# Optimization experiments

Hardware: AMD Instinct MI355X
Metric: run time of the kernel (lower is better)

Reference implementation:

```python
import jax, jax.numpy as jnp
import numpy as np
import math

B, S, H, M, NH = 4, 1024, 1024, 32768, 1  # batch, seq, hidden, memory_size, num_heads


def setup_inputs() -> dict:
    key = jax.random.key(0)
    ks = jax.random.split(key, 12)
    init = lambda k, shape: (jax.random.normal(k, shape, dtype=jnp.float32) * 0.02)
    return {
        "hidden_states": jax.random.normal(ks[0], (B, S, H), dtype=jnp.float32),
        "Wq": init(ks[1], (H, H)), "bq": jnp.zeros((H,), jnp.float32),
        "Wk": init(ks[2], (H, H)), "bk": jnp.zeros((H,), jnp.float32),
        "Wv": init(ks[3], (H, H)), "bv": jnp.zeros((H,), jnp.float32),
        "Wo": init(ks[4], (H, H)), "bo": jnp.zeros((H,), jnp.float32),
        "memory_keys": init(ks[5], (NH, M, H)),
        "memory_values": init(ks[6], (NH, M, H)),
        "memory_age": jnp.zeros((NH, M), jnp.float32),
    }


def reference(hidden_states, Wq, bq, Wk, bk, Wv, bv, Wo, bo,
              memory_keys, memory_values, memory_age):
    b, s, _ = hidden_states.shape
    # projections (torch Linear: x @ W.T + b), split into heads
    q = (hidden_states @ Wq.T + bq).reshape(b, s, NH, -1)
    k = (hidden_states @ Wk.T + bk).reshape(b, s, NH, -1)
    v = (hidden_states @ Wv.T + bv).reshape(b, s, NH, -1)

    # cross-attention to external memory: [b,s,h,m]
    scores = jnp.einsum('bshd,hmd->bshm', q, memory_keys) / math.sqrt(H)
    probs = jax.nn.softmax(scores, axis=-1)  # dropout is identity (eval / p used deterministically)
    mem_out = jnp.einsum('bshm,hmd->bshd', probs, memory_values)

    # --- memory update (LRU-style topk scatter) ---
    age = memory_age + 1.0                       # [h,m]
    importance = probs.sum(axis=(0, 1))          # [h,m]
    _, upd_idx = jax.lax.top_k(age + (1.0 - importance), s)  # [h, s]
    h_idx = jnp.arange(NH)[:, None]              # [h,1]
    src_k = k[0, -1][:, None, :]                 # [h,1,d] -> broadcast over s slots
    src_v = v[0, -1][:, None, :]
    new_keys = memory_keys.at[h_idx, upd_idx].set(src_k)
    new_values = memory_values.at[h_idx, upd_idx].set(src_v)
    new_age = age.at[h_idx, upd_idx].set(0.0)

    output = mem_out.reshape(b, s, -1) @ Wo.T + bo

    access_counts = jnp.sum(probs > 0.01, axis=(0, 1))          # [h,m]
    max_scores = jnp.max(scores, axis=-1).mean()
    memory_usage = jnp.mean((new_age > 0).astype(jnp.float32))
    return (output, access_counts, max_scores, memory_usage,
            new_keys, new_values, new_age)
```

## Files before the change

### kernel.cpp

```cpp
#include <hip/hip_runtime.h>

#define SCALE 0.03125f
#define BAND_EPS 1e-6
#define BAND_CAP 8192
#define RB 4
#define NCHUNK 8

typedef unsigned int u32;
typedef unsigned short u16;
typedef unsigned long long u64;
typedef __attribute__((ext_vector_type(8))) short bf16x8;
typedef __attribute__((ext_vector_type(4))) float f32x4;

#define MFMA16(A,B,C) __builtin_amdgcn_mfma_f32_16x16x32_bf16(A,B,C,0,0,0)

__device__ __forceinline__ u32 fenc(float x){ u32 u=__float_as_uint(x); return (u&0x80000000u)? ~u : (u|0x80000000u); }
__device__ __forceinline__ float fdec(u32 e){ return (e&0x80000000u)? __uint_as_float(e&0x7FFFFFFFu) : __uint_as_float(~e); }
__device__ __forceinline__ u16 f2bf(float f){ u32 u=__float_as_uint(f); u32 r=(u + 0x7FFFu + ((u>>16)&1u))>>16; return (u16)r; }
__device__ __forceinline__ float bf2f(u16 h){ return __uint_as_float(((u32)h)<<16); }

__device__ __forceinline__ uint4 nt_load16(const void* p){
  const u64* q = (const u64*)p;
  u64 lo = __builtin_nontemporal_load(q);
  u64 hi = __builtin_nontemporal_load(q+1);
  uint4 r;
  r.x = (u32)lo; r.y = (u32)(lo>>32);
  r.z = (u32)hi; r.w = (u32)(hi>>32);
  return r;
}

__global__ __launch_bounds__(256) void k_projq64(const float* __restrict__ X, const float* __restrict__ W,
    const float* __restrict__ bias, float* __restrict__ Qhi, u16* __restrict__ Qh, u16* __restrict__ Ql)
{
  __shared__ float Xs[16][68], Ws[16][68];
  int t=threadIdx.x, ty=t>>4, tx=t&15;
  int row0=blockIdx.y*64, col0=blockIdx.x*64;
  int lr=t>>2, lk=(t&3)*4;
  double acc[4][4]={};
  for (int k0=0;k0<1024;k0+=16){
    __syncthreads();
    {
      float4 x = *(const float4*)(X + (size_t)(row0+lr)*1024 + k0 + lk);
      float4 w = *(const float4*)(W + (size_t)(col0+lr)*1024 + k0 + lk);
      Xs[lk+0][lr]=x.x; Xs[lk+1][lr]=x.y; Xs[lk+2][lr]=x.z; Xs[lk+3][lr]=x.w;
      Ws[lk+0][lr]=w.x; Ws[lk+1][lr]=w.y; Ws[lk+2][lr]=w.z; Ws[lk+3][lr]=w.w;
    }
    __syncthreads();
    #pragma unroll
    for (int kk=0;kk<16;kk++){
      double a[4], b[4];
      #pragma unroll
      for (int i=0;i<4;i++) a[i] = (double)Xs[kk][ty*4+i];
      #pragma unroll
      for (int j=0;j<4;j++) b[j] = (double)Ws[kk][tx*4+j];
      #pragma unroll
      for (int i=0;i<4;i++)
        #pragma unroll
        for (int j=0;j<4;j++)
          acc[i][j] = fma(a[i], b[j], acc[i][j]);
    }
  }
  #pragma unroll
  for (int i=0;i<4;i++)
    #pragma unroll
    for (int j=0;j<4;j++){
      double q = acc[i][j] + (double)bias[col0+tx*4+j];
      float hi = (float)q;
      size_t off = (size_t)(row0+ty*4+i)*1024 + col0 + tx*4 + j;
      Qhi[off] = hi;
      if (Qh){
        u16 h = f2bf(hi);
        Qh[off] = h;
        Ql[off] = f2bf(hi - bf2f(h));
      }
    }
}

__global__ __launch_bounds__(256) void k_rowproj(const float* __restrict__ hs,
    const float* __restrict__ Wk, const float* __restrict__ bk,
    const float* __restrict__ Wv, const float* __restrict__ bv,
    float* __restrict__ krow, float* __restrict__ vrow)
{
  int b = blockIdx.x; int which = b >> 10; int o = b & 1023; int t = threadIdx.x;
  const float* W = which ? Wv : Wk;
  const float* bias = which ? bv : bk;
  const float* x = hs + (size_t)1023*1024;
  double s = 0;
  for (int k=t;k<1024;k+=256) s += (double)x[k] * (double)W[(size_t)o*1024+k];
  __shared__ double sd[256];
  sd[t]=s; __syncthreads();
  for (int off=128;off>0;off>>=1){ if(t<off) sd[t]+=sd[t+off]; __syncthreads(); }
  if (t==0){ float* dst = which? vrow : krow; dst[o] = (float)(sd[0] + (double)bias[o]); }
}

__global__ __launch_bounds__(256) void k_cvt_mk(const float* __restrict__ src, u16* __restrict__ dst)
{
  size_t base = ((size_t)blockIdx.x*256 + threadIdx.x) * 16;
  float v[16];
  #pragma unroll
  for (int q=0;q<4;q++) *(float4*)&v[q*4] = *(const float4*)(src + base + q*4);
  u16 h[16];
  #pragma unroll
  for (int q=0;q<16;q++) h[q] = f2bf(v[q]);
  *(uint4*)(dst+base)   = *(uint4*)&h[0];
  *(uint4*)(dst+base+8) = *(uint4*)&h[8];
}

__global__ __launch_bounds__(256) void k_cvt_mvt(const float* __restrict__ MV, u32* __restrict__ MVT)
{
  size_t mp = blockIdx.x; int d = threadIdx.x*4;
  float4 r0 = *(const float4*)(MV + (2*mp  )*1024 + d);
  float4 r1 = *(const float4*)(MV + (2*mp+1)*1024 + d);
  u32 o[4];
  o[0] = (u32)f2bf(r0.x) | ((u32)f2bf(r1.x)<<16);
  o[1] = (u32)f2bf(r0.y) | ((u32)f2bf(r1.y)<<16);
  o[2] = (u32)f2bf(r0.z) | ((u32)f2bf(r1.z)<<16);
  o[3] = (u32)f2bf(r0.w) | ((u32)f2bf(r1.w)<<16);
  *(uint4*)(MVT + mp*1024 + d) = *(uint4*)o;
}

template<bool SPLIT>
__device__ __forceinline__ void sweep_core(
    const float* __restrict__ Qg, const float* __restrict__ MKg,
    int row0, int col0,
    u16 (*Ah)[40], u16 (*Al)[40], u16 (*Bh)[40],
    f32x4 acc[2][8])
{
  int t = threadIdx.x;
  int w = t >> 6, g = (t >> 4) & 3, c = t & 15;
  int srow = t >> 1, sq = (t & 1) * 16;
  const float* xg = Qg  + (size_t)(row0 + srow)*1024 + sq;
  const float* wg = MKg + (size_t)(col0 + srow)*1024 + sq;
  float xr[16], wr[16];
  #pragma unroll
  for (int q=0;q<4;q++){
    *(float4*)&xr[q*4] = *(const float4*)(xg + q*4);
    *(float4*)&wr[q*4] = *(const float4*)(wg + q*4);
  }
  for (int k0 = 0; k0 < 1024; k0 += 32){
    u16 ah[16], al[16], bh[16];
    #pragma unroll
    for (int q=0;q<16;q++){
      u16 h = f2bf(xr[q]); ah[q]=h;
      bh[q] = f2bf(wr[q]);
      if constexpr (SPLIT) al[q]=f2bf(xr[q]-bf2f(h));
    }
    __syncthreads();
    *(uint4*)&Ah[srow][sq]   = *(uint4*)&ah[0];
    *(uint4*)&Ah[srow][sq+8] = *(uint4*)&ah[8];
    *(uint4*)&Bh[srow][sq]   = *(uint4*)&bh[0];
    *(uint4*)&Bh[srow][sq+8] = *(uint4*)&bh[8];
    if constexpr (SPLIT){
      *(uint4*)&Al[srow][sq]   = *(uint4*)&al[0];
      *(uint4*)&Al[srow][sq+8] = *(uint4*)&al[8];
    }
    __syncthreads();
    if (k0 + 32 < 1024){
      #pragma unroll
      for (int q=0;q<4;q++){
        *(float4*)&xr[q*4] = *(const float4*)(xg + k0+32 + q*4);
        *(float4*)&wr[q*4] = *(const float4*)(wg + k0+32 + q*4);
      }
    }
    bf16x8 afh[2], afl[2];
    #pragma unroll
    for (int fi=0; fi<2; fi++){
      afh[fi] = *(const bf16x8*)&Ah[w*32 + fi*16 + c][g*8];
      if constexpr (SPLIT) afl[fi] = *(const bf16x8*)&Al[w*32 + fi*16 + c][g*8];
    }
    #pragma unroll
    for (int fj=0; fj<8; fj++){
      bf16x8 bfh = *(const bf16x8*)&Bh[fj*16 + c][g*8];
      #pragma unroll
      for (int fi=0; fi<2; fi++){
        acc[fi][fj] = MFMA16(afh[fi], bfh, acc[fi][fj]);
        if constexpr (SPLIT)
          acc[fi][fj] = MFMA16(afl[fi], bfh, acc[fi][fj]);
      }
    }
  }
}

template<bool SPLIT>
__device__ __forceinline__ void sweep_core_pre(
    const u16* __restrict__ Ag, const u16* __restrict__ Alg, const u16* __restrict__ Bg,
    int row0, int col0,
    u16 (*Ah)[40], u16 (*Al)[40], u16 (*Bh)[40],
    f32x4 acc[2][8])
{
  int t = threadIdx.x;
  int w = t >> 6, g = (t >> 4) & 3, c = t & 15;
  int srow = t >> 1, sq = (t & 1) * 16;
  const u16* xa = Ag + (size_t)(row0+srow)*1024 + sq;
  const u16* wb = Bg + (size_t)(col0+srow)*1024 + sq;
  const u16* xl = Alg + (size_t)(row0+srow)*1024 + sq;
  uint4 a0 = *(const uint4*)xa, a1 = *(const uint4*)(xa+8);
  uint4 b0 = *(const uint4*)wb, b1 = *(const uint4*)(wb+8);
  uint4 l0, l1;
  if constexpr (SPLIT){ l0 = *(const uint4*)xl; l1 = *(const uint4*)(xl+8); }
  for (int k0 = 0; k0 < 1024; k0 += 32){
    __syncthreads();
    *(uint4*)&Ah[srow][sq]   = a0;
    *(uint4*)&Ah[srow][sq+8] = a1;
    *(uint4*)&Bh[srow][sq]   = b0;
    *(uint4*)&Bh[srow][sq+8] = b1;
    if constexpr (SPLIT){
      *(uint4*)&Al[srow][sq]   = l0;
      *(uint4*)&Al[srow][sq+8] = l1;
    }
    __syncthreads();
    if (k0 + 32 < 1024){
      a0=*(const uint4*)(xa+k0+32); a1=*(const uint4*)(xa+k0+40);
      b0=*(const uint4*)(wb+k0+32); b1=*(const uint4*)(wb+k0+40);
      if constexpr (SPLIT){ l0=*(const uint4*)(xl+k0+32); l1=*(const uint4*)(xl+k0+40); }
    }
    bf16x8 afh[2], afl[2];
    #pragma unroll
    for (int fi=0; fi<2; fi++){
      afh[fi] = *(const bf16x8*)&Ah[w*32 + fi*16 + c][g*8];
      if constexpr (SPLIT) afl[fi] = *(const bf16x8*)&Al[w*32 + fi*16 + c][g*8];
    }
    #pragma unroll
    for (int fj=0; fj<8; fj++){
      bf16x8 bfh = *(const bf16x8*)&Bh[fj*16 + c][g*8];
      #pragma unroll
      for (int fi=0; fi<2; fi++){
        acc[fi][fj] = MFMA16(afh[fi], bfh, acc[fi][fj]);
        if constexpr (SPLIT)
          acc[fi][fj] = MFMA16(afl[fi], bfh, acc[fi][fj]);
      }
    }
  }
}

__device__ __forceinline__ void sweep1_epi(f32x4 acc[2][8], int row0,
    double* Zrow, u32* rmk)
{
  int t=threadIdx.x, w=t>>6, g=(t>>4)&3, c=t&15;
  #pragma unroll
  for (int fi=0;fi<2;fi++){
    #pragma unroll
    for (int r=0;r<4;r++){
      float mx=-1e30f, sm=0.f;
      #pragma unroll
      for (int fj=0;fj<8;fj++){
        float sc = acc[fi][fj][r]*SCALE;
        mx = fmaxf(mx, sc);
        sm += expf(sc);
      }
      #pragma unroll
      for (int o=1;o<16;o<<=1){
        mx = fmaxf(mx, __shfl_xor(mx,o,64));
        sm += __shfl_xor(sm,o,64);
      }
      if (c==0){
        int row = row0 + w*32 + fi*16 + g*4 + r;
        atomicMax(&rmk[row], fenc(mx));
        atomicAdd(&Zrow[row], (double)sm);
      }
    }
  }
}

__global__ __launch_bounds__(256) void k_sweep1m(const float* __restrict__ Q,
    const float* __restrict__ MK, double* __restrict__ Zrow, u32* __restrict__ rmk)
{
  __shared__ __align__(16) u16 ldsbuf[2*128*40];
  u16 (*Ah)[40]=(u16(*)[40])(ldsbuf);
  u16 (*Bh)[40]=(u16(*)[40])(ldsbuf+128*40);
  int row0=blockIdx.y*128, col0=blockIdx.x*128;
  f32x4 acc[2][8];
  #pragma unroll
  for (int fi=0;fi<2;fi++)
    #pragma unroll
    for (int fj=0;fj<8;fj++) acc[fi][fj] = (f32x4){0.f,0.f,0.f,0.f};
  sweep_core<false>(Q, MK, row0, col0, Ah, Ah, Bh, acc);
  sweep1_epi(acc, row0, Zrow, rmk);
}

__global__ __launch_bounds__(256) void k_sweep1p(const u16* __restrict__ Qh,
    const u16* __restrict__ MKh, double* __restrict__ Zrow, u32* __restrict__ rmk)
{
  __shared__ __align__(16) u16 ldsbuf[2*128*40];
  u16 (*Ah)[40]=(u16(*)[40])(ldsbuf);
  u16 (*Bh)[40]=(u16(*)[40])(ldsbuf+128*40);
  int row0=blockIdx.y*128, col0=blockIdx.x*128;
  f32x4 acc[2][8];
  #pragma unroll
  for (int fi=0;fi<2;fi++)
    #pragma unroll
    for (int fj=0;fj<8;fj++) acc[fi][fj] = (f32x4){0.f,0.f,0.f,0.f};
  sweep_core_pre<false>(Qh, Qh, MKh, row0, col0, Ah, Ah, Bh, acc);
  sweep1_epi(acc, row0, Zrow, rmk);
}

__global__ __launch_bounds__(256) void k_invz(const double* __restrict__ Z, const u32* __restrict__ rmk,
    float* __restrict__ invZ, double* __restrict__ invZd, float* __restrict__ rowmax)
{
  int r = blockIdx.x*256 + threadIdx.x;
  double iz = 1.0 / Z[r];
  invZ[r] = (float)iz;
  invZd[r] = iz;
  rowmax[r] = fdec(rmk[r]);
}

__device__ __forceinline__ void sweep2_epi(f32x4 acc[2][8], int row0, int col0,
    const float* invZ, double* imp, int* cnt, u16* P, u16* ldsbuf)
{
  int t=threadIdx.x, w=t>>6, g=(t>>4)&3, c=t&15;
  double colp[8]={0,0,0,0,0,0,0,0};
  int    colc[8]={0,0,0,0,0,0,0,0};
  #pragma unroll
  for (int fi=0;fi<2;fi++){
    float iz[4];
    #pragma unroll
    for (int r=0;r<4;r++) iz[r] = invZ[row0 + w*32 + fi*16 + g*4 + r];
    #pragma unroll
    for (int fj=0;fj<8;fj++){
      #pragma unroll
      for (int r=0;r<4;r++){
        float p = expf(acc[fi][fj][r]*SCALE)*iz[r];
        int row = row0 + w*32 + fi*16 + g*4 + r;
        __builtin_nontemporal_store(f2bf(p), &P[(size_t)row*32768 + col0 + fj*16 + c]);
        colp[fj] += (double)p;
        colc[fj] += (p > 0.01f) ? 1 : 0;
      }
    }
  }
  __syncthreads();
  double (*red)[128] = (double(*)[128])ldsbuf;
  #pragma unroll
  for (int fj=0;fj<8;fj++) red[w*4+g][fj*16+c] = colp[fj];
  __syncthreads();
  if (t < 128){
    double s=0;
    #pragma unroll
    for (int q=0;q<16;q++) s += red[q][t];
    atomicAdd(&imp[col0+t], s);
  }
  __syncthreads();
  #pragma unroll
  for (int fj=0;fj<8;fj++) red[w*4+g][fj*16+c] = (double)colc[fj];
  __syncthreads();
  if (t < 128){
    double s=0;
    #pragma unroll
    for (int q=0;q<16;q++) s += red[q][t];
    int ci = (int)(s+0.5);
    if (ci) atomicAdd(&cnt[col0+t], ci);
  }
}

__global__ __launch_bounds__(256) void k_sweep2m(const float* __restrict__ Q,
    const float* __restrict__ MK, const float* __restrict__ invZ,
    double* __restrict__ imp, int* __restrict__ cnt, u16* __restrict__ P)
{
  __shared__ __align__(16) u16 ldsbuf[3*128*40];
  u16 (*Ah)[40]=(u16(*)[40])(ldsbuf);
  u16 (*Al)[40]=(u16(*)[40])(ldsbuf+128*40);
  u16 (*Bh)[40]=(u16(*)[40])(ldsbuf+2*128*40);
  int row0=blockIdx.y*128, col0=blockIdx.x*128;
  f32x4 acc[2][8];
  #pragma unroll
  for (int fi=0;fi<2;fi++)
    #pragma unroll
    for (int fj=0;fj<8;fj++) acc[fi][fj] = (f32x4){0.f,0.f,0.f,0.f};
  sweep_core<true>(Q, MK, row0, col0, Ah, Al, Bh, acc);
  sweep2_epi(acc, row0, col0, invZ, imp, cnt, P, ldsbuf);
}

__global__ __launch_bounds__(256) void k_sweep2p(const u16* __restrict__ Qh,
    const u16* __restrict__ Ql, const u16* __restrict__ MKh, const float* __restrict__ invZ,
    double* __restrict__ imp, int* __restrict__ cnt, u16* __restrict__ P)
{
  __shared__ __align__(16) u16 ldsbuf[3*128*40];
  u16 (*Ah)[40]=(u16(*)[40])(ldsbuf);
  u16 (*Al)[40]=(u16(*)[40])(ldsbuf+128*40);
  u16 (*Bh)[40]=(u16(*)[40])(ldsbuf+2*128*40);
  int row0=blockIdx.y*128, col0=blockIdx.x*128;
  f32x4 acc[2][8];
  #pragma unroll
  for (int fi=0;fi<2;fi++)
    #pragma unroll
    for (int fj=0;fj<8;fj++) acc[fi][fj] = (f32x4){0.f,0.f,0.f,0.f};
  sweep_core_pre<true>(Qh, Ql, MKh, row0, col0, Ah, Al, Bh, acc);
  sweep2_epi(acc, row0, col0, invZ, imp, cnt, P, ldsbuf);
}

template<int MODE>
__global__ __launch_bounds__(1024) void k_select(const double* __restrict__ imp,
    const float* __restrict__ mage, double* __restrict__ vsout, int* __restrict__ sel)
{
  __shared__ int hist[256];
  __shared__ int scanbuf[1024];
  __shared__ u32 s_digit; __shared__ int s_rr;
  int t = threadIdx.x;
  int m0 = t*32;
  u32 key[32];
  #pragma unroll
  for (int i=0;i<32;i++){
    int m = m0+i;
    float v = (mage[m] + 1.0f) + (1.0f - (float)imp[m]);
    key[i] = fenc(v);
  }
  u32 prefix = 0, pmask = 0;
  int rr = 1024;
  for (int pass=0; pass<4; pass++){
    int shift = 24 - pass*8;
    if (t<256) hist[t]=0;
    __syncthreads();
    #pragma unroll
    for (int i=0;i<32;i++){
      if ((key[i] & pmask) == prefix)
        atomicAdd(&hist[(key[i]>>shift)&255u], 1);
    }
    __syncthreads();
    if (t==0){
      int cum=0; int d=255;
      for (; d>0; d--){
        if (cum + hist[d] >= rr) break;
        cum += hist[d];
      }
      s_rr = rr - cum;
      s_digit = (u32)d;
    }
    __syncthreads();
    rr = s_rr;
    prefix |= (s_digit << shift);
    pmask  |= (255u << shift);
    __syncthreads();
  }
  u32 keystar = prefix;
  int krem = rr;
  if (MODE==0){
    if (t==0) *vsout = (double)fdec(keystar);
    return;
  }
  int lc = 0;
  #pragma unroll
  for (int i=0;i<32;i++) lc += (key[i]==keystar) ? 1 : 0;
  scanbuf[t] = lc;
  __syncthreads();
  for (int off=1; off<1024; off<<=1){
    int v_ = scanbuf[t];
    int add = (t>=off)? scanbuf[t-off] : 0;
    __syncthreads();
    scanbuf[t] = v_ + add;
    __syncthreads();
  }
  int run = scanbuf[t] - lc;
  #pragma unroll
  for (int i=0;i<32;i++){
    int s_;
    if (key[i] > keystar) s_ = 1;
    else if (key[i] == keystar){ s_ = (run < krem) ? 1 : 0; run++; }
    else s_ = 0;
    sel[m0+i] = s_;
  }
}

__global__ __launch_bounds__(256) void k_band(const double* __restrict__ imp,
    const float* __restrict__ mage, const double* __restrict__ vsp,
    int* __restrict__ bandcnt, int* __restrict__ bandidx)
{
  int m = blockIdx.x*256 + threadIdx.x;
  double v = ((double)mage[m] + 1.0) + (1.0 - imp[m]);
  double vs = *vsp;
  if (fabs(v - vs) <= BAND_EPS){
    int idx = atomicAdd(bandcnt, 1);
    if (idx < BAND_CAP) bandidx[idx] = m;
  }
}

__global__ __launch_bounds__(256) void k_repair2(const int* __restrict__ bandcnt, const int* __restrict__ bandidx,
    const float* __restrict__ Qhi, const float* __restrict__ MK,
    const double* __restrict__ invZd, double* __restrict__ partial)
{
  int bc = *bandcnt; if (bc > BAND_CAP) bc = BAND_CAP;
  int s0 = blockIdx.x * RB;
  if (s0 >= bc) return;
  int ns = bc - s0; if (ns > RB) ns = RB;
  int r0 = blockIdx.y * 512;
  __shared__ float mks[RB][1024];
  __shared__ double izl[512];
  __shared__ double red[256];
  int t = threadIdx.x;
  for (int idx = t; idx < RB*1024; idx += 256){
    int j = idx >> 10, d = idx & 1023;
    mks[j][d] = (j < ns) ? MK[(size_t)bandidx[s0+j]*1024 + d] : 0.f;
  }
  for (int r = t; r < 512; r += 256) izl[r] = invZd[r0 + r];
  __syncthreads();
  int wave = t>>6, lane = t&63, d0 = lane*16, sl = lane&3;
  double mkr[RB][16];
  #pragma unroll
  for (int j=0;j<RB;j++)
    #pragma unroll
    for (int q=0;q<16;q++) mkr[j][q] = (double)mks[j][d0+q];
  double acc = 0;
  for (int rr = wave; rr < 512; rr += 4){
    const float4* hp = (const float4*)(Qhi + (size_t)(r0+rr)*1024 + d0);
    float4 h0=hp[0], h1=hp[1], h2=hp[2], h3=hp[3];
    double hh[16]={h0.x,h0.y,h0.z,h0.w,h1.x,h1.y,h1.z,h1.w,
                   h2.x,h2.y,h2.z,h2.w,h3.x,h3.y,h3.z,h3.w};
    double p[RB];
    #pragma unroll
    for (int j=0;j<RB;j++){
      double a0=0, a1=0;
      #pragma unroll
      for (int q=0;q<8;q++){
        a0 = fma(hh[2*q],   mkr[j][2*q],   a0);
        a1 = fma(hh[2*q+1], mkr[j][2*q+1], a1);
      }
      p[j] = a0 + a1;
    }
    #pragma unroll
    for (int o=1;o<16;o<<=1)
      #pragma unroll
      for (int j=0;j<RB;j++) p[j] += __shfl_xor(p[j], o, 64);
    double v = (sl==0)? p[0] : (sl==1)? p[1] : (sl==2)? p[2] : p[3];
    v += __shfl_xor(v, 16, 64);
    v += __shfl_xor(v, 32, 64);
    acc += exp(v * (1.0/32.0)) * izl[rr];
  }
  red[t] = acc;
  __syncthreads();
  for (int o=128; o>=RB; o>>=1){
    if (t < o) red[t] += red[t+o];
    __syncthreads();
  }
  if (t < ns) partial[(size_t)(s0+t)*NCHUNK + blockIdx.y] = red[t];
}

__global__ __launch_bounds__(256) void k_repair_fin(const int* __restrict__ bandcnt,
    const int* __restrict__ bandidx, const double* __restrict__ partial, double* __restrict__ imp)
{
  int bc = *bandcnt; if (bc > BAND_CAP) bc = BAND_CAP;
  int slot = blockIdx.x*256 + threadIdx.x;
  if (slot >= bc) return;
  double s = 0;
  #pragma unroll
  for (int ch=0; ch<NCHUNK; ch++) s += partial[(size_t)slot*NCHUNK + ch];
  imp[bandidx[slot]] = s * 0.0625;
}

__global__ __launch_bounds__(256) void k_pvm(const u16* __restrict__ P,
    const float* __restrict__ MV, float* __restrict__ O)
{
  __shared__ __align__(16) u16 Ap[128][40];
  __shared__ u32 Bv[16][132];
  int t=threadIdx.x, w=t>>6, g=(t>>4)&3, c=t&15;
  int row0=blockIdx.x*128, d0=blockIdx.y*128;
  size_t kb0 = (size_t)blockIdx.z*8192;
  int srow=t>>1, sq=(t&1)*16;
  int mp=t>>5, dc=t&31;
  f32x4 acc[2][8];
  #pragma unroll
  for (int fi=0;fi<2;fi++)
    #pragma unroll
    for (int fj=0;fj<8;fj++) acc[fi][fj] = (f32x4){0.f,0.f,0.f,0.f};
  const u16*  pg  = P  + (size_t)(row0+srow)*32768 + kb0 + sq;
  const float* mva = MV + (kb0 + 2*mp  )*1024 + d0 + dc;
  const float* mvb = mva + 1024;
  const float* mvc = mva + 16*1024;
  const float* mvd = mvc + 1024;
  uint4 pa0 = *(const uint4*)pg;
  uint4 pa1 = *(const uint4*)(pg + 8);
  float a0[4], b0[4], a1[4], b1[4];
  #pragma unroll
  for (int j=0;j<4;j++){ a0[j]=mva[32*j]; b0[j]=mvb[32*j]; a1[j]=mvc[32*j]; b1[j]=mvd[32*j]; }
  for (int kt=0; kt<256; kt++){
    __syncthreads();
    *(uint4*)&Ap[srow][sq]   = pa0;
    *(uint4*)&Ap[srow][sq+8] = pa1;
    #pragma unroll
    for (int j=0;j<4;j++){
      Bv[mp  ][dc+32*j] = (u32)f2bf(a0[j]) | ((u32)f2bf(b0[j])<<16);
      Bv[mp+8][dc+32*j] = (u32)f2bf(a1[j]) | ((u32)f2bf(b1[j])<<16);
    }
    __syncthreads();
    if (kt+1 < 256){
      size_t ko = (size_t)(kt+1)*32;
      pa0 = *(const uint4*)(pg + ko);
      pa1 = *(const uint4*)(pg + ko + 8);
      size_t fo = ko*1024;
      #pragma unroll
      for (int j=0;j<4;j++){
        a0[j]=mva[fo+32*j]; b0[j]=mvb[fo+32*j];
        a1[j]=mvc[fo+32*j]; b1[j]=mvd[fo+32*j];
      }
    }
    bf16x8 af[2];
    af[0] = *(const bf16x8*)&Ap[w*32 + c][g*8];
    af[1] = *(const bf16x8*)&Ap[w*32 + 16 + c][g*8];
    #pragma unroll
    for (int fj=0; fj<8; fj++){
      union { u32 u[4]; bf16x8 v; } bb;
      #pragma unroll
      for (int qq=0; qq<4; qq++) bb.u[qq] = Bv[4*g+qq][fj*16 + c];
      acc[0][fj] = MFMA16(af[0], bb.v, acc[0][fj]);
      acc[1][fj] = MFMA16(af[1], bb.v, acc[1][fj]);
    }
  }
  #pragma unroll
  for (int fi=0;fi<2;fi++)
    #pragma unroll
    for (int fj=0;fj<8;fj++)
      #pragma unroll
      for (int r=0;r<4;r++)
        atomicAdd(&O[(size_t)(row0 + w*32 + fi*16 + g*4 + r)*1024 + d0 + fj*16 + c],
                  acc[fi][fj][r]);
}

__global__ __launch_bounds__(256) void k_pvmp(const u16* __restrict__ P,
    const u32* __restrict__ MVT, float* __restrict__ O)
{
  __shared__ __align__(16) u16 Ap[128][40];
  __shared__ u32 Bv[16][132];
  int t=threadIdx.x, w=t>>6, g=(t>>4)&3, c=t&15;
  int row0=blockIdx.x*128, d0=blockIdx.y*128;
  size_t kb0 = (size_t)blockIdx.z*8192;
  size_t pb0 = kb0 >> 1;
  int srow=t>>1, sq=(t&1)*16;
  int mp=t>>5, dc=t&31;
  f32x4 acc[2][8];
  #pragma unroll
  for (int fi=0;fi<2;fi++)
    #pragma unroll
    for (int fj=0;fj<8;fj++) acc[fi][fj] = (f32x4){0.f,0.f,0.f,0.f};
  const u16* pg   = P   + (size_t)(row0+srow)*32768 + kb0 + sq;
  const u32* mvt0 = MVT + (pb0 + mp    )*1024 + d0 + dc;
  const u32* mvt1 = MVT + (pb0 + 8 + mp)*1024 + d0 + dc;
  uint4 pa0 = nt_load16(pg);
  uint4 pa1 = nt_load16(pg + 8);
  u32 b0[4], b1[4];
  #pragma unroll
  for (int j=0;j<4;j++){ b0[j]=mvt0[32*j]; b1[j]=mvt1[32*j]; }
  for (int kt=0; kt<256; kt++){
    __syncthreads();
    *(uint4*)&Ap[srow][sq]   = pa0;
    *(uint4*)&Ap[srow][sq+8] = pa1;
    #pragma unroll
    for (int j=0;j<4;j++){
      Bv[mp  ][dc+32*j] = b0[j];
      Bv[mp+8][dc+32*j] = b1[j];
    }
    __syncthreads();
    if (kt+1 < 256){
      size_t ko = (size_t)(kt+1)*32;
      pa0 = nt_load16(pg + ko);
      pa1 = nt_load16(pg + ko + 8);
      size_t fo = (size_t)(kt+1)*16*1024;
      #pragma unroll
      for (int j=0;j<4;j++){ b0[j]=mvt0[fo+32*j]; b1[j]=mvt1[fo+32*j]; }
    }
    bf16x8 af[2];
    af[0] = *(const bf16x8*)&Ap[w*32 + c][g*8];
    af[1] = *(const bf16x8*)&Ap[w*32 + 16 + c][g*8];
    #pragma unroll
    for (int fj=0; fj<8; fj++){
      union { u32 u[4]; bf16x8 v; } bb;
      #pragma unroll
      for (int qq=0; qq<4; qq++) bb.u[qq] = Bv[4*g+qq][fj*16 + c];
      acc[0][fj] = MFMA16(af[0], bb.v, acc[0][fj]);
      acc[1][fj] = MFMA16(af[1], bb.v, acc[1][fj]);
    }
  }
  #pragma unroll
  for (int fi=0;fi<2;fi++)
    #pragma unroll
    for (int fj=0;fj<8;fj++)
      #pragma unroll
      for (int r=0;r<4;r++)
        atomicAdd(&O[(size_t)(row0 + w*32 + fi*16 + g*4 + r)*1024 + d0 + fj*16 + c],
                  acc[fi][fj][r]);
}

__global__ __launch_bounds__(256) void k_projm(const float* __restrict__ X,
    const float* __restrict__ W, const float* __restrict__ bias, float* __restrict__ Y)
{
  __shared__ __align__(16) u16 ldsbuf[2*128*40];
  u16 (*Ah)[40]=(u16(*)[40])(ldsbuf);
  u16 (*Bh)[40]=(u16(*)[40])(ldsbuf+128*40);
  int t=threadIdx.x, w=t>>6, g=(t>>4)&3, c=t&15;
  int row0=blockIdx.y*128, col0=blockIdx.x*128;
  f32x4 acc[2][8];
  #pragma unroll
  for (int fi=0;fi<2;fi++)
    #pragma unroll
    for (int fj=0;fj<8;fj++) acc[fi][fj] = (f32x4){0.f,0.f,0.f,0.f};
  sweep_core<false>(X, W, row0, col0, Ah, Ah, Bh, acc);
  #pragma unroll
  for (int fi=0;fi<2;fi++)
    #pragma unroll
    for (int fj=0;fj<8;fj++){
      float bb = bias[col0 + fj*16 + c];
      #pragma unroll
      for (int r=0;r<4;r++)
        Y[(size_t)(row0 + w*32 + fi*16 + g*4 + r)*1024 + col0 + fj*16 + c]
          = acc[fi][fj][r] + bb;
    }
}

__global__ __launch_bounds__(256) void k_scatter(const float* __restrict__ mk, const float* __restrict__ mv,
    const float* __restrict__ mage, const float* __restrict__ krow, const float* __restrict__ vrow,
    const int* __restrict__ sel, float* __restrict__ nk, float* __restrict__ nv,
    float* __restrict__ na, int* __restrict__ usage)
{
  int s = blockIdx.x, t = threadIdx.x;
  bool is = sel[s] != 0;
  const float2* sk = (const float2*)krow;
  const float2* sv = (const float2*)vrow;
  const float2* ok = (const float2*)(mk + (size_t)s*1024);
  const float2* ov = (const float2*)(mv + (size_t)s*1024);
  float2* dk = (float2*)(nk + (size_t)s*1024);
  float2* dv = (float2*)(nv + (size_t)s*1024);
  #pragma unroll
  for (int q=t;q<512;q+=256){
    dk[q] = is ? sk[q] : ok[q];
    dv[q] = is ? sv[q] : ov[q];
  }
  if (t==0){
    float a = mage[s] + 1.0f;
    float nav = is ? 0.0f : a;
    na[s] = nav;
    if (nav > 0.0f) atomicAdd(usage, 1);
  }
}

__global__ __launch_bounds__(256) void k_fin(const float* __restrict__ rowmax, const int* __restrict__ cnt,
    const int* __restrict__ usage, float* __restrict__ acc_out, float* __restrict__ scal)
{
  int t = threadIdx.x;
  __shared__ double sd[256];
  double s = 0;
  for (int r=t;r<4096;r+=256) s += (double)rowmax[r];
  sd[t]=s; __syncthreads();
  for (int o=128;o>0;o>>=1){ if (t<o) sd[t]+=sd[t+o]; __syncthreads(); }
  if (t==0){
    scal[0] = (float)(sd[0] / 4096.0);
    scal[1] = (float)((double)(*usage) / 32768.0);
  }
  for (int m=t;m<32768;m+=256) acc_out[m] = (float)cnt[m];
}

extern "C" void kernel_launch(void* const* d_in, const int* in_sizes, int n_in,
                              void* d_out, int out_size, void* d_ws, size_t ws_size,
                              hipStream_t stream) {
  const float* hs  = (const float*)d_in[0];
  const float* Wq  = (const float*)d_in[1];
  const float* bq  = (const float*)d_in[2];
  const float* Wk  = (const float*)d_in[3];
  const float* bk  = (const float*)d_in[4];
  const float* Wv  = (const float*)d_in[5];
  const float* bv  = (const float*)d_in[6];
  const float* Wo  = (const float*)d_in[7];
  const float* bo  = (const float*)d_in[8];
  const float* mk  = (const float*)d_in[9];
  const float* mv  = (const float*)d_in[10];
  const float* mage= (const float*)d_in[11];
  float* out = (float*)d_out;

  char* ws = (char*)d_ws;
  const size_t MB = 1024*1024;
  bool fast = ws_size >= 82*MB;
  size_t stats_off = fast ? 80*MB : 16*MB;
  char* st = ws + stats_off;

  double* Zrow   = (double*)(st);
  u32*    rmk    = (u32*)  (st + 32768);
  float*  invZ   = (float*)(st + 49152);
  double* invZd  = (double*)(st + 65536);
  float*  rowmax = (float*)(st + 98304);
  double* imp    = (double*)(st + 114688);
  int*    cnt    = (int*)  (st + 376832);
  int*    sel    = (int*)  (st + 507904);
  float*  krow   = (float*)(st + 638976);
  float*  vrow   = (float*)(st + 643072);
  int*    usage  = (int*)  (st + 647168);
  double* vstar  = (double*)(st + 647176);
  int*    bandcnt= (int*)  (st + 647184);
  int*    bandidx= (int*)  (st + 647188);
  double* partial= (double*)(st + 680960);

  float* O   = (float*)ws;
  u16*   Qh  = (u16*)ws;
  u16*   Ql  = (u16*)(ws + 8*MB);
  u16*   MKh = (u16*)(ws + 16*MB);
  u32*   MVT = (u32*)(ws + 16*MB);

  float* Qhi = (float*)d_out;
  u16*   P   = (u16*)((char*)d_out + 16908544);

  dim3 blk(256);
  if (fast){
    hipMemsetAsync(st, 0, 647188 + BAND_CAP*4, stream);
    k_projq64<<<dim3(16,64),blk,0,stream>>>(hs, Wq, bq, Qhi, Qh, Ql);
    k_cvt_mk<<<8192,blk,0,stream>>>(mk, MKh);
    k_rowproj<<<2048,blk,0,stream>>>(hs, Wk, bk, Wv, bv, krow, vrow);
    k_sweep1p<<<dim3(256,32),blk,0,stream>>>(Qh, MKh, Zrow, rmk);
    k_invz<<<16,blk,0,stream>>>(Zrow, rmk, invZ, invZd, rowmax);
    k_sweep2p<<<dim3(256,32),blk,0,stream>>>(Qh, Ql, MKh, invZ, imp, cnt, P);
    hipMemsetAsync(ws, 0, 16*MB, stream);
    k_cvt_mvt<<<16384,blk,0,stream>>>(mv, MVT);
    k_select<0><<<1,1024,0,stream>>>(imp, mage, vstar, nullptr);
    k_band<<<128,blk,0,stream>>>(imp, mage, vstar, bandcnt, bandidx);
    k_repair2<<<dim3(BAND_CAP/RB, NCHUNK),blk,0,stream>>>(bandcnt, bandidx, Qhi, mk, invZd, partial);
    k_repair_fin<<<BAND_CAP/256,blk,0,stream>>>(bandcnt, bandidx, partial, imp);
    k_pvmp<<<dim3(32,8,4),blk,0,stream>>>(P, MVT, O);
    k_projm<<<dim3(8,32),blk,0,stream>>>(O, Wo, bo, out);
    k_select<1><<<1,1024,0,stream>>>(imp, mage, nullptr, sel);
    k_scatter<<<32768,blk,0,stream>>>(mk, mv, mage, krow, vrow, sel,
        out + 4227074, out + 37781506, out + 71335938, usage);
    k_fin<<<1,blk,0,stream>>>(rowmax, cnt, usage, out + 4194304, out + 4227072);
  } else {
    hipMemsetAsync(ws, 0, 16*MB + 647188 + BAND_CAP*4, stream);
    k_projq64<<<dim3(16,64),blk,0,stream>>>(hs, Wq, bq, Qhi, nullptr, nullptr);
    k_rowproj<<<2048,blk,0,stream>>>(hs, Wk, bk, Wv, bv, krow, vrow);
    k_sweep1m<<<dim3(256,32),blk,0,stream>>>(Qhi, mk, Zrow, rmk);
    k_invz<<<16,blk,0,stream>>>(Zrow, rmk, invZ, invZd, rowmax);
    k_sweep2m<<<dim3(256,32),blk,0,stream>>>(Qhi, mk, invZ, imp, cnt, P);
    k_select<0><<<1,1024,0,stream>>>(imp, mage, vstar, nullptr);
    k_band<<<128,blk,0,stream>>>(imp, mage, vstar, bandcnt, bandidx);
    k_repair2<<<dim3(BAND_CAP/RB, NCHUNK),blk,0,stream>>>(bandcnt, bandidx, Qhi, mk, invZd, partial);
    k_repair_fin<<<BAND_CAP/256,blk,0,stream>>>(bandcnt, bandidx, partial, imp);
    k_pvm<<<dim3(32,8,4),blk,0,stream>>>(P, mv, O);
    k_projm<<<dim3(8,32),blk,0,stream>>>(O, Wo, bo, out);
    k_select<1><<<1,1024,0,stream>>>(imp, mage, nullptr, sel);
    k_scatter<<<32768,blk,0,stream>>>(mk, mv, mage, krow, vrow, sel,
        out + 4227074, out + 37781506, out + 71335938, usage);
    k_fin<<<1,blk,0,stream>>>(rowmax, cnt, usage, out + 4194304, out + 4227072);
  }
}
```

Before: 2.917 ms.

## Double-buffer LDS and remap block order in P·V kernel

The P×V bf16 MFMA kernel now uses two LDS buffers with a two-stage register prefetch. This removes one of the two barriers per k-step and lets global loads for step k+2 overlap compute on step k. The launch becomes a 1D grid, and block indices are swizzled so that consecutive blocks are spread across XCDs, which should improve L2 reuse of P and MVT tiles. The cost is doubled LDS use and more registers, which may lower occupancy.

```diff
diff --git a/kernel.cpp b/kernel.cpp
--- a/kernel.cpp
+++ b/kernel.cpp
@@ -615,11 +615,14 @@
 __global__ __launch_bounds__(256) void k_pvmp(const u16* __restrict__ P,
     const u32* __restrict__ MVT, float* __restrict__ O)
 {
-  __shared__ __align__(16) u16 Ap[128][40];
-  __shared__ u32 Bv[16][132];
+  __shared__ __align__(16) u16 Ap[2][128][40];
+  __shared__ u32 Bv[2][16][132];
   int t=threadIdx.x, w=t>>6, g=(t>>4)&3, c=t&15;
-  int row0=blockIdx.x*128, d0=blockIdx.y*128;
-  size_t kb0 = (size_t)blockIdx.z*8192;
+  int l = blockIdx.x;
+  int lsw = (l & 7)*128 + (l >> 3);
+  int bx = lsw & 31, by = (lsw >> 5) & 7, bz = lsw >> 8;
+  int row0 = bx*128, d0 = by*128;
+  size_t kb0 = (size_t)bz*8192;
   size_t pb0 = kb0 >> 1;
   int srow=t>>1, sq=(t&1)*16;
   int mp=t>>5, dc=t&31;
@@ -631,41 +634,47 @@
   const u16* pg   = P   + (size_t)(row0+srow)*32768 + kb0 + sq;
   const u32* mvt0 = MVT + (pb0 + mp    )*1024 + d0 + dc;
   const u32* mvt1 = MVT + (pb0 + 8 + mp)*1024 + d0 + dc;
-  uint4 pa0 = nt_load16(pg);
-  uint4 pa1 = nt_load16(pg + 8);
-  u32 b0[4], b1[4];
-  #pragma unroll
-  for (int j=0;j<4;j++){ b0[j]=mvt0[32*j]; b1[j]=mvt1[32*j]; }
+
+  uint4 pa0[2], pa1[2];
+  u32 vb0[2][4], vb1[2][4];
+  #define LOADSET(s, kt) { \
+    size_t ko = (size_t)(kt)*32; \
+    pa0[s] = nt_load16(pg + ko); \
+    pa1[s] = nt_load16(pg + ko + 8); \
+    size_t fo = (size_t)(kt)*16*1024; \
+    _Pragma("unroll") \
+    for (int j=0;j<4;j++){ vb0[s][j]=mvt0[fo+32*j]; vb1[s][j]=mvt1[fo+32*j]; } }
+  #define WRITEBUF(b, s) { \
+    *(uint4*)&Ap[b][srow][sq]   = pa0[s]; \
+    *(uint4*)&Ap[b][srow][sq+8] = pa1[s]; \
+    _Pragma("unroll") \
+    for (int j=0;j<4;j++){ \
+      Bv[b][mp  ][dc+32*j] = vb0[s][j]; \
+      Bv[b][mp+8][dc+32*j] = vb1[s][j]; } }
+
+  LOADSET(0, 0);
+  LOADSET(1, 1);
+  WRITEBUF(0, 0);
+  __syncthreads();
   for (int kt=0; kt<256; kt++){
-    __syncthreads();
-    *(uint4*)&Ap[srow][sq]   = pa0;
-    *(uint4*)&Ap[srow][sq+8] = pa1;
-    #pragma unroll
-    for (int j=0;j<4;j++){
-      Bv[mp  ][dc+32*j] = b0[j];
-      Bv[mp+8][dc+32*j] = b1[j];
-    }
-    __syncthreads();
-    if (kt+1 < 256){
-      size_t ko = (size_t)(kt+1)*32;
-      pa0 = nt_load16(pg + ko);
-      pa1 = nt_load16(pg + ko + 8);
-      size_t fo = (size_t)(kt+1)*16*1024;
-      #pragma unroll
-      for (int j=0;j<4;j++){ b0[j]=mvt0[fo+32*j]; b1[j]=mvt1[fo+32*j]; }
-    }
+    int cur = kt & 1, nxt = cur ^ 1;
+    if (kt+2 < 256) LOADSET(cur, kt+2);
+    if (kt+1 < 256) WRITEBUF(nxt, nxt);
     bf16x8 af[2];
-    af[0] = *(const bf16x8*)&Ap[w*32 + c][g*8];
-    af[1] = *(const bf16x8*)&Ap[w*32 + 16 + c][g*8];
+    af[0] = *(const bf16x8*)&Ap[cur][w*32 + c][g*8];
+    af[1] = *(const bf16x8*)&Ap[cur][w*32 + 16 + c][g*8];
     #pragma unroll
     for (int fj=0; fj<8; fj++){
       union { u32 u[4]; bf16x8 v; } bb;
       #pragma unroll
-      for (int qq=0; qq<4; qq++) bb.u[qq] = Bv[4*g+qq][fj*16 + c];
+      for (int qq=0; qq<4; qq++) bb.u[qq] = Bv[cur][4*g+qq][fj*16 + c];
       acc[0][fj] = MFMA16(af[0], bb.v, acc[0][fj]);
       acc[1][fj] = MFMA16(af[1], bb.v, acc[1][fj]);
     }
-  }
+    __syncthreads();
+  }
+  #undef LOADSET
+  #undef WRITEBUF
   #pragma unroll
   for (int fi=0;fi<2;fi++)
     #pragma unroll
@@ -807,7 +816,7 @@
     k_band<<<128,blk,0,stream>>>(imp, mage, vstar, bandcnt, bandidx);
     k_repair2<<<dim3(BAND_CAP/RB, NCHUNK),blk,0,stream>>>(bandcnt, bandidx, Qhi, mk, invZd, partial);
     k_repair_fin<<<BAND_CAP/256,blk,0,stream>>>(bandcnt, bandidx, partial, imp);
-    k_pvmp<<<dim3(32,8,4),blk,0,stream>>>(P, MVT, O);
+    k_pvmp<<<1024,blk,0,stream>>>(P, MVT, O);
     k_projm<<<dim3(8,32),blk,0,stream>>>(O, Wo, bo, out);
     k_select<1><<<1,1024,0,stream>>>(imp, mage, nullptr, sel);
     k_scatter<<<32768,blk,0,stream>>>(mk, mv, mage, krow, vrow, sel,
```

New measurement: 3.572 ms. +22.5%, slower.
